# Optimization experiments

Hardware: AMD Instinct MI355X
Metric: run time of the kernel (lower is better)

Reference implementation:

```python
import jax, jax.numpy as jnp
import numpy as np

D_MODEL = 512
N_HEADS = 8
D_K = D_MODEL // N_HEADS
D_EDGE = 16
D_FF = 2048
B, N = 4, 1024
LN_EPS = 1e-5


def layer_norm(x, g, b):
    mu = jnp.mean(x, axis=-1, keepdims=True)
    var = jnp.var(x, axis=-1, keepdims=True)
    return (x - mu) * jax.lax.rsqrt(var + LN_EPS) * g + b


def setup_inputs() -> dict:
    key = jax.random.key(0)
    ks = jax.random.split(key, 16)
    s = 0.02
    return {
        "x": jax.random.normal(ks[0], (B, N, D_MODEL), jnp.float32),
        "edge_emb": jax.random.normal(ks[1], (B, N, N, D_EDGE), jnp.float32),
        "mask": jnp.ones((B, N), dtype=bool),
        # attention weights (torch Linear layout: [out, in])
        "wq": jax.random.normal(ks[2], (D_MODEL, D_MODEL), jnp.float32) * s,
        "wk": jax.random.normal(ks[3], (D_MODEL, D_MODEL), jnp.float32) * s,
        "wv": jax.random.normal(ks[4], (D_MODEL, D_MODEL), jnp.float32) * s,
        "wo": jax.random.normal(ks[5], (D_MODEL, D_MODEL), jnp.float32) * s,
        "wo_b": jnp.zeros((D_MODEL,), jnp.float32),
        # edge bias projector
        "we": jax.random.normal(ks[6], (N_HEADS, D_EDGE), jnp.float32) * s,
        "we_b": jnp.zeros((N_HEADS,), jnp.float32),
        # layer norms
        "g1": jnp.ones((D_MODEL,), jnp.float32),
        "b1n": jnp.zeros((D_MODEL,), jnp.float32),
        "g2": jnp.ones((D_MODEL,), jnp.float32),
        "b2n": jnp.zeros((D_MODEL,), jnp.float32),
        # FFN
        "w1": jax.random.normal(ks[7], (D_FF, D_MODEL), jnp.float32) * s,
        "b1": jnp.zeros((D_FF,), jnp.float32),
        "w2": jax.random.normal(ks[8], (D_MODEL, D_FF), jnp.float32) * s,
        "b2": jnp.zeros((D_MODEL,), jnp.float32),
    }


def reference(x, edge_emb, mask, wq, wk, wv, wo, wo_b, we, we_b,
              g1, b1n, g2, b2n, w1, b1, w2, b2):
    Bx, n, D = x.shape
    H, d_k = N_HEADS, D // N_HEADS
    residual = x
    xn = layer_norm(x, g1, b1n)
    # [B, H, n, d_k]
    Q = (xn @ wq.T).reshape(Bx, n, H, d_k).transpose(0, 2, 1, 3)
    K = (xn @ wk.T).reshape(Bx, n, H, d_k).transpose(0, 2, 1, 3)
    V = (xn @ wv.T).reshape(Bx, n, H, d_k).transpose(0, 2, 1, 3)
    scale = 1.0 / jnp.sqrt(jnp.asarray(d_k, x.dtype))
    attn = jnp.einsum('bhid,bhjd->bhij', Q, K) * scale  # [B, H, n, n]
    # per-head additive edge bias: [B, n, n, H] -> [B, H, n, n]
    bias = (edge_emb @ we.T + we_b).transpose(0, 3, 1, 2)
    attn = attn + bias
    attn = jnp.where(mask[:, None, None, :], attn, -jnp.inf)
    attn = jax.nn.softmax(attn, axis=-1)
    attn = jnp.nan_to_num(attn, nan=0.0)  # fully-masked rows -> 0
    out = jnp.einsum('bhij,bhjd->bhid', attn, V)
    out = out.transpose(0, 2, 1, 3).reshape(Bx, n, D)
    out = out @ wo.T + wo_b
    x = residual + out
    xn2 = layer_norm(x, g2, b2n)
    h = jax.nn.gelu(xn2 @ w1.T + b1, approximate=False)  # torch nn.GELU default = exact
    x = x + (h @ w2.T + b2)
    return x
```

## Files before the change

### kernel.cpp

```cpp
#include <hip/hip_runtime.h>
#include <math.h>

#define D_MODEL 512
#define N_HEADS 8
#define D_K     64
#define D_EDGE  16
#define D_FF    2048
#define B_SZ    4
#define N_SEQ   1024
#define M_ROWS  (B_SZ * N_SEQ)
#define LN_EPS  1e-5f
#define JSPLIT  4
#define ROWS_T  (B_SZ * N_HEADS * N_SEQ)

typedef __attribute__((ext_vector_type(4))) float f32x4;
typedef __attribute__((ext_vector_type(8))) short s16x8;
typedef __attribute__((ext_vector_type(8))) unsigned short u16x8;
typedef __attribute__((ext_vector_type(4))) unsigned short u16x4;

__device__ __forceinline__ unsigned short f2bf(float f) {
  union { float f; unsigned u; } x; x.f = f;
  unsigned r = x.u + 0x7fffu + ((x.u >> 16) & 1u);
  return (unsigned short)(r >> 16);
}
__device__ __forceinline__ float bf2f(unsigned short u) {
  union { unsigned u; float f; } x; x.u = ((unsigned)u) << 16;
  return x.f;
}
__device__ __forceinline__ float gelu_exact(float v) {
  return 0.5f * v * (1.0f + erff(v * 0.70710678118654752440f));
}

__global__ __launch_bounds__(256) void cast_weights(
    const float* __restrict__ wq, const float* __restrict__ wk, const float* __restrict__ wv,
    const float* __restrict__ wo, const float* __restrict__ w1, const float* __restrict__ w2,
    unsigned short* __restrict__ wbf)
{
  const int i4 = blockIdx.x * 256 + threadIdx.x;
  const float* src; int off4;
  if (i4 < 196608) {
    const int sub = i4 >> 16;
    src = (sub == 0) ? wq : ((sub == 1) ? wk : wv);
    off4 = i4 & 65535;
  } else if (i4 < 262144) { src = wo; off4 = i4 - 196608; }
  else if (i4 < 524288)   { src = w1; off4 = i4 - 262144; }
  else                    { src = w2; off4 = i4 - 524288; }
  const float4 v = ((const float4*)src)[off4];
  u16x4 p = { f2bf(v.x), f2bf(v.y), f2bf(v.z), f2bf(v.w) };
  *(u16x4*)(wbf + (size_t)i4 * 4) = p;
}

__global__ __launch_bounds__(256) void ln_kernel(
    const float* __restrict__ x, const float* __restrict__ g,
    const float* __restrict__ bb, unsigned short* __restrict__ out)
{
  const int row  = blockIdx.x * 4 + (threadIdx.x >> 6);
  const int lane = threadIdx.x & 63;
  const float4* xr = (const float4*)(x + (size_t)row * D_MODEL);
  float4 v0 = xr[lane * 2 + 0];
  float4 v1 = xr[lane * 2 + 1];
  float s  = v0.x + v0.y + v0.z + v0.w + v1.x + v1.y + v1.z + v1.w;
  float ss = v0.x*v0.x + v0.y*v0.y + v0.z*v0.z + v0.w*v0.w
           + v1.x*v1.x + v1.y*v1.y + v1.z*v1.z + v1.w*v1.w;
  #pragma unroll
  for (int off = 32; off >= 1; off >>= 1) {
    s  += __shfl_xor(s, off);
    ss += __shfl_xor(ss, off);
  }
  const float mu  = s * (1.0f / D_MODEL);
  const float var = ss * (1.0f / D_MODEL) - mu * mu;
  const float r   = rsqrtf(var + LN_EPS);
  const float4* gp = (const float4*)g;
  const float4* bp = (const float4*)bb;
  float4 g0 = gp[lane*2+0], g1v = gp[lane*2+1];
  float4 b0 = bp[lane*2+0], b1v = bp[lane*2+1];
  u16x4 oa = { f2bf((v0.x - mu) * r * g0.x + b0.x),
               f2bf((v0.y - mu) * r * g0.y + b0.y),
               f2bf((v0.z - mu) * r * g0.z + b0.z),
               f2bf((v0.w - mu) * r * g0.w + b0.w) };
  u16x4 ob = { f2bf((v1.x - mu) * r * g1v.x + b1v.x),
               f2bf((v1.y - mu) * r * g1v.y + b1v.y),
               f2bf((v1.z - mu) * r * g1v.z + b1v.z),
               f2bf((v1.w - mu) * r * g1v.w + b1v.w) };
  unsigned short* orow = out + (size_t)row * D_MODEL + lane * 8;
  *(u16x4*)(orow)     = oa;
  *(u16x4*)(orow + 4) = ob;
}

template<int ACT, int RES, int OBF, int HB>
__global__ __launch_bounds__(256, 4) void gemm_bf16(
    const unsigned short* __restrict__ A, const unsigned short* __restrict__ W,
    const float* __restrict__ bias, const float* __restrict__ res,
    void* __restrict__ Cv, int Nout, int K)
{
  __shared__ unsigned short As[128 * 64];
  __shared__ unsigned short Ws[64 * 64];
  const int tid  = threadIdx.x;
  const int w    = tid >> 6;
  const int lane = tid & 63;
  const int g    = lane >> 4;
  const int c    = lane & 15;
  const int row0 = blockIdx.x * 128;
  const int col0 = blockIdx.y * 64;
  const f32x4 z = { 0.f, 0.f, 0.f, 0.f };
  f32x4 acc[2][4];
  #pragma unroll
  for (int fm = 0; fm < 2; ++fm)
    #pragma unroll
    for (int fn = 0; fn < 4; ++fn) acc[fm][fn] = z;

  for (int k0 = 0; k0 < K; k0 += 64) {
    #pragma unroll
    for (int i = 0; i < 4; ++i) {
      const int flat = i * 256 + tid;
      __builtin_amdgcn_global_load_lds(
          (const __attribute__((address_space(1))) void*)(A + (size_t)(row0 + (flat >> 3)) * K + k0 + (flat & 7) * 8),
          (__attribute__((address_space(3))) void*)(&As[flat * 8]), 16, 0, 0);
    }
    #pragma unroll
    for (int i = 0; i < 2; ++i) {
      const int flat = i * 256 + tid;
      __builtin_amdgcn_global_load_lds(
          (const __attribute__((address_space(1))) void*)(W + (size_t)(col0 + (flat >> 3)) * K + k0 + (flat & 7) * 8),
          (__attribute__((address_space(3))) void*)(&Ws[flat * 8]), 16, 0, 0);
    }
    __syncthreads();
    #pragma unroll
    for (int kk = 0; kk < 2; ++kk) {
      const s16x8 a0 = *(const s16x8*)&As[(w * 32 + c) * 64 + kk * 32 + 8 * g];
      const s16x8 a1 = *(const s16x8*)&As[(w * 32 + 16 + c) * 64 + kk * 32 + 8 * g];
      #pragma unroll
      for (int fn = 0; fn < 4; ++fn) {
        const s16x8 bfr = *(const s16x8*)&Ws[(fn * 16 + c) * 64 + kk * 32 + 8 * g];
        acc[0][fn] = __builtin_amdgcn_mfma_f32_16x16x32_bf16(a0, bfr, acc[0][fn], 0, 0, 0);
        acc[1][fn] = __builtin_amdgcn_mfma_f32_16x16x32_bf16(a1, bfr, acc[1][fn], 0, 0, 0);
      }
    }
    __syncthreads();
  }

  #pragma unroll
  for (int fn = 0; fn < 4; ++fn) {
    const int cc = col0 + fn * 16 + c;
    const float bv = HB ? bias[cc] : 0.0f;
    #pragma unroll
    for (int fm = 0; fm < 2; ++fm) {
      #pragma unroll
      for (int r = 0; r < 4; ++r) {
        const int rr = row0 + w * 32 + fm * 16 + 4 * g + r;
        float v = acc[fm][fn][r] + bv;
        if (ACT) v = gelu_exact(v);
        if (RES) v += res[(size_t)rr * Nout + cc];
        if (OBF) ((unsigned short*)Cv)[(size_t)rr * Nout + cc] = f2bf(v);
        else     ((float*)Cv)[(size_t)rr * Nout + cc] = v;
      }
    }
  }
}

__global__ __launch_bounds__(256) void transpose_v(
    const unsigned short* __restrict__ qkv, unsigned short* __restrict__ vT)
{
  const int bid = blockIdx.x;
  const int jt = bid & 15, h = (bid >> 4) & 7, b = bid >> 7;
  __shared__ unsigned short t[64][72];
  const int tid = threadIdx.x;
  #pragma unroll
  for (int itr = 0; itr < 2; ++itr) {
    const int flat = itr * 256 + tid;
    const int j = flat >> 3, ch = flat & 7;
    *(u16x8*)&t[j][ch * 8] =
        *(const u16x8*)(qkv + (size_t)(b * 1024 + jt * 64 + j) * 1536 + 1024 + h * 64 + ch * 8);
  }
  __syncthreads();
  #pragma unroll
  for (int itr = 0; itr < 2; ++itr) {
    const int flat = itr * 256 + tid;
    const int dd = flat >> 3, ch = flat & 7;
    u16x8 v;
    #pragma unroll
    for (int e = 0; e < 8; ++e) v[e] = t[ch * 8 + e][dd];
    *(u16x8*)(vT + (size_t)((b * 8 + h) * 64 + dd) * 1024 + jt * 64 + ch * 8) = v;
  }
}

__global__ __launch_bounds__(512, 4) void attn_kernel(
    const unsigned short* __restrict__ qkv, const unsigned short* __restrict__ vT,
    const float* __restrict__ edge, const unsigned char* __restrict__ mask,
    const float* __restrict__ we, const float* __restrict__ web,
    float* __restrict__ pm, float* __restrict__ pl, float* __restrict__ pacc)
{
  __shared__ unsigned short bias_s[8][32][40];
  __shared__ unsigned short p_s[8][32][40];
  __shared__ float we_s[8][16];
  __shared__ float web_s[8];

  const int bid   = blockIdx.x;
  const int b     = (bid & 7) >> 1;
  const int local = ((bid >> 3) << 1) | (bid & 1);
  const int split = local & 3;
  const int it    = local >> 2;
  const int i0    = it * 32;
  const int tid   = threadIdx.x;
  const int h     = tid >> 6;
  const int lane  = tid & 63;
  const int g     = lane >> 4;
  const int c     = lane & 15;

  if (tid < 128) we_s[tid >> 4][tid & 15] = we[tid];
  if (tid < 8)   web_s[tid] = web[tid];

  s16x8 qf[2][2];
  #pragma unroll
  for (int fm = 0; fm < 2; ++fm)
    #pragma unroll
    for (int kk = 0; kk < 2; ++kk)
      qf[fm][kk] = *(const s16x8*)(qkv + (size_t)(b * 1024 + i0 + fm * 16 + c) * 1536 + h * 64 + kk * 32 + 8 * g);

  const f32x4 z = { 0.f, 0.f, 0.f, 0.f };
  f32x4 o[2][4];
  #pragma unroll
  for (int fm = 0; fm < 2; ++fm)
    #pragma unroll
    for (int fd = 0; fd < 4; ++fd) o[fm][fd] = z;
  float mreg[2][4], lreg[2][4];
  #pragma unroll
  for (int fm = 0; fm < 2; ++fm)
    #pragma unroll
    for (int r = 0; r < 4; ++r) { mreg[fm][r] = -1e30f; lreg[fm][r] = 0.f; }

  for (int jc = 0; jc < 8; ++jc) {
    const int j0 = split * 256 + jc * 32;
    __syncthreads();
    {
      const int pi  = tid >> 4;
      const int pjb = (tid & 15) * 2;
      #pragma unroll
      for (int pp = 0; pp < 2; ++pp) {
        const int pj = pjb + pp;
        const int j  = j0 + pj;
        const float4* ep = (const float4*)(edge +
            ((((size_t)b * N_SEQ) + (i0 + pi)) * N_SEQ + j) * D_EDGE);
        const float4 e0 = ep[0], e1 = ep[1], e2 = ep[2], e3 = ep[3];
        const float mk = mask[b * N_SEQ + j] ? 0.0f : -1e30f;
        #pragma unroll
        for (int hh = 0; hh < 8; ++hh) {
          const float* wv = we_s[hh];
          const float d =
              e0.x*wv[0]  + e0.y*wv[1]  + e0.z*wv[2]  + e0.w*wv[3]
            + e1.x*wv[4]  + e1.y*wv[5]  + e1.z*wv[6]  + e1.w*wv[7]
            + e2.x*wv[8]  + e2.y*wv[9]  + e2.z*wv[10] + e2.w*wv[11]
            + e3.x*wv[12] + e3.y*wv[13] + e3.z*wv[14] + e3.w*wv[15];
          bias_s[hh][pi][pj] = f2bf(d + web_s[hh] + mk);
        }
      }
    }
    __syncthreads();

    f32x4 s[2][2];
    s[0][0] = z; s[0][1] = z; s[1][0] = z; s[1][1] = z;
    #pragma unroll
    for (int fn = 0; fn < 2; ++fn)
      #pragma unroll
      for (int kk = 0; kk < 2; ++kk) {
        const s16x8 kf = *(const s16x8*)(qkv +
            (size_t)(b * 1024 + j0 + fn * 16 + c) * 1536 + 512 + h * 64 + kk * 32 + 8 * g);
        #pragma unroll
        for (int fm = 0; fm < 2; ++fm)
          s[fm][fn] = __builtin_amdgcn_mfma_f32_16x16x32_bf16(qf[fm][kk], kf, s[fm][fn], 0, 0, 0);
      }

    #pragma unroll
    for (int fm = 0; fm < 2; ++fm) {
      #pragma unroll
      for (int r = 0; r < 4; ++r) {
        const int irow = fm * 16 + 4 * g + r;
        const float s0 = s[fm][0][r] * 0.125f + bf2f(bias_s[h][irow][c]);
        const float s1 = s[fm][1][r] * 0.125f + bf2f(bias_s[h][irow][16 + c]);
        float v = fmaxf(s0, s1);
        v = fmaxf(v, __shfl_xor(v, 1));
        v = fmaxf(v, __shfl_xor(v, 2));
        v = fmaxf(v, __shfl_xor(v, 4));
        v = fmaxf(v, __shfl_xor(v, 8));
        const float nm    = fmaxf(mreg[fm][r], v);
        const float alpha = __expf(mreg[fm][r] - nm);
        mreg[fm][r] = nm;
        const float p0 = __expf(s0 - nm);
        const float p1 = __expf(s1 - nm);
        lreg[fm][r] = lreg[fm][r] * alpha + p0 + p1;
        #pragma unroll
        for (int fd = 0; fd < 4; ++fd) o[fm][fd][r] *= alpha;
        p_s[h][irow][c]      = f2bf(p0);
        p_s[h][irow][16 + c] = f2bf(p1);
      }
    }

    s16x8 pa[2];
    #pragma unroll
    for (int fm = 0; fm < 2; ++fm)
      pa[fm] = *(const s16x8*)&p_s[h][fm * 16 + c][8 * g];
    #pragma unroll
    for (int fd = 0; fd < 4; ++fd) {
      const s16x8 vf = *(const s16x8*)(vT +
          (size_t)((b * 8 + h) * 64 + fd * 16 + c) * 1024 + j0 + 8 * g);
      #pragma unroll
      for (int fm = 0; fm < 2; ++fm)
        o[fm][fd] = __builtin_amdgcn_mfma_f32_16x16x32_bf16(pa[fm], vf, o[fm][fd], 0, 0, 0);
    }
  }

  #pragma unroll
  for (int fm = 0; fm < 2; ++fm) {
    #pragma unroll
    for (int r = 0; r < 4; ++r) {
      float lv = lreg[fm][r];
      lv += __shfl_xor(lv, 1);
      lv += __shfl_xor(lv, 2);
      lv += __shfl_xor(lv, 4);
      lv += __shfl_xor(lv, 8);
      const int row = ((split * B_SZ + b) * N_HEADS + h) * N_SEQ + i0 + fm * 16 + 4 * g + r;
      #pragma unroll
      for (int fd = 0; fd < 4; ++fd)
        pacc[(size_t)row * 64 + fd * 16 + c] = o[fm][fd][r];
      if (c == 0) { pm[row] = mreg[fm][r]; pl[row] = lv; }
    }
  }
}

__global__ __launch_bounds__(256) void merge_kernel(
    const float* __restrict__ pm, const float* __restrict__ pl,
    const float* __restrict__ pacc, unsigned short* __restrict__ ao)
{
  const int row = blockIdx.x * 4 + (threadIdx.x >> 6);
  const int d   = threadIdx.x & 63;
  float ms[JSPLIT], ls[JSPLIT];
  float M = -3e38f;
  #pragma unroll
  for (int s2 = 0; s2 < JSPLIT; ++s2) {
    ms[s2] = pm[s2 * ROWS_T + row];
    ls[s2] = pl[s2 * ROWS_T + row];
    M = fmaxf(M, ms[s2]);
  }
  float acc = 0.f, inv = 0.f;
  if (M > -1e29f) {
    float L = 0.f;
    #pragma unroll
    for (int s2 = 0; s2 < JSPLIT; ++s2) {
      const float wgt = __expf(ms[s2] - M);
      L += ls[s2] * wgt;
      acc += wgt * pacc[((size_t)s2 * ROWS_T + row) * 64 + d];
    }
    inv = 1.0f / L;
  }
  const int b2 = row >> 13, h2 = (row >> 10) & 7, i2 = row & 1023;
  ao[(size_t)(b2 * 1024 + i2) * 512 + h2 * 64 + d] = f2bf(acc * inv);
}

extern "C" void kernel_launch(void* const* d_in, const int* in_sizes, int n_in,
                              void* d_out, int out_size, void* d_ws, size_t ws_size,
                              hipStream_t stream) {
  const float* x    = (const float*)d_in[0];
  const float* edge = (const float*)d_in[1];
  const unsigned char* mask = (const unsigned char*)d_in[2];
  const float* wq   = (const float*)d_in[3];
  const float* wk   = (const float*)d_in[4];
  const float* wv   = (const float*)d_in[5];
  const float* wo   = (const float*)d_in[6];
  const float* wo_b = (const float*)d_in[7];
  const float* we   = (const float*)d_in[8];
  const float* we_b = (const float*)d_in[9];
  const float* g1   = (const float*)d_in[10];
  const float* b1n  = (const float*)d_in[11];
  const float* g2   = (const float*)d_in[12];
  const float* b2n  = (const float*)d_in[13];
  const float* w1   = (const float*)d_in[14];
  const float* b1   = (const float*)d_in[15];
  const float* w2   = (const float*)d_in[16];
  const float* b2   = (const float*)d_in[17];
  float* out = (float*)d_out;
  char* ws = (char*)d_ws;

  const size_t MB = 1048576;
  unsigned short* xn_bf  = (unsigned short*)(ws + 0 * MB);
  unsigned short* qkv_bf = (unsigned short*)(ws + 4 * MB);
  unsigned short* vT     = (unsigned short*)(ws + 16 * MB);
  unsigned short* ao_bf  = (unsigned short*)(ws + 20 * MB);
  float*          x2     = (float*)(ws + 24 * MB);
  unsigned short* wbf    = (unsigned short*)(ws + 32 * MB);
  float*          pm     = (float*)(ws + 38 * MB);
  float*          pl     = (float*)(ws + 38 * MB + 524288);
  float*          pacc   = (float*)(ws + 41 * MB);
  unsigned short* hbuf   = (unsigned short*)(ws + 41 * MB);

  unsigned short* wqkv_bf = wbf;
  unsigned short* wo_bf   = wbf + 786432;
  unsigned short* w1_bf   = wbf + 1048576;
  unsigned short* w2_bf   = wbf + 2097152;

  cast_weights<<<3072, 256, 0, stream>>>(wq, wk, wv, wo, w1, w2, wbf);
  ln_kernel<<<M_ROWS / 4, 256, 0, stream>>>(x, g1, b1n, xn_bf);
  {
    dim3 grid(M_ROWS / 128, 1536 / 64);
    gemm_bf16<0, 0, 1, 0><<<grid, 256, 0, stream>>>(xn_bf, wqkv_bf, nullptr, nullptr, qkv_bf, 1536, 512);
  }
  transpose_v<<<512, 256, 0, stream>>>(qkv_bf, vT);
  attn_kernel<<<512, 512, 0, stream>>>(qkv_bf, vT, edge, mask, we, we_b, pm, pl, pacc);
  merge_kernel<<<ROWS_T / 4, 256, 0, stream>>>(pm, pl, pacc, ao_bf);
  {
    dim3 grid(M_ROWS / 128, 512 / 64);
    gemm_bf16<0, 1, 0, 1><<<grid, 256, 0, stream>>>(ao_bf, wo_bf, wo_b, x, (void*)x2, 512, 512);
  }
  ln_kernel<<<M_ROWS / 4, 256, 0, stream>>>(x2, g2, b2n, xn_bf);
  {
    dim3 grid(M_ROWS / 128, 2048 / 64);
    gemm_bf16<1, 0, 1, 1><<<grid, 256, 0, stream>>>(xn_bf, w1_bf, b1, nullptr, hbuf, 2048, 512);
  }
  {
    dim3 grid(M_ROWS / 128, 512 / 64);
    gemm_bf16<0, 1, 0, 1><<<grid, 256, 0, stream>>>(hbuf, w2_bf, b2, x2, (void*)out, 512, 2048);
  }
}
```

Before: 587.4 us.

## Halve attention row tile, prefetch edge features, add 64x64 GEMM for narrow outputs

The attention kernel now handles 16 query rows per block instead of 32, doubling the grid to 1024 blocks. The next chunk's edge embedding is prefetched into registers while the current chunk is processed, and the jc loop is fully unrolled. A new 64x64-tile GEMM using global_load_lds feeds the two 512-wide output projections (Wo and W2) to raise block count and occupancy. In exchange, per-block K/V reuse drops in attention and the new GEMM has no double-buffering.

After: 587.9 us. Within noise of the previous version (+0.1%).

```diff
diff --git a/kernel.cpp b/kernel.cpp
--- a/kernel.cpp
+++ b/kernel.cpp
@@ -158,6 +158,76 @@
   }
 }
 
+template<int ACT, int RES, int OBF, int HB>
+__global__ __launch_bounds__(256, 4) void gemm64_bf16(
+    const unsigned short* __restrict__ A, const unsigned short* __restrict__ W,
+    const float* __restrict__ bias, const float* __restrict__ res,
+    void* __restrict__ Cv, int Nout, int K)
+{
+  __shared__ unsigned short As[64 * 64];
+  __shared__ unsigned short Ws[64 * 64];
+  const int tid  = threadIdx.x;
+  const int w    = tid >> 6;
+  const int lane = tid & 63;
+  const int g    = lane >> 4;
+  const int c    = lane & 15;
+  const int wr   = (w >> 1) * 32;
+  const int wc   = (w & 1) * 32;
+  const int row0 = blockIdx.x * 64;
+  const int col0 = blockIdx.y * 64;
+  const f32x4 z = { 0.f, 0.f, 0.f, 0.f };
+  f32x4 acc[2][2];
+  acc[0][0] = z; acc[0][1] = z; acc[1][0] = z; acc[1][1] = z;
+
+  for (int k0 = 0; k0 < K; k0 += 64) {
+    #pragma unroll
+    for (int i = 0; i < 2; ++i) {
+      const int flat = i * 256 + tid;
+      __builtin_amdgcn_global_load_lds(
+          (const __attribute__((address_space(1))) void*)(A + (size_t)(row0 + (flat >> 3)) * K + k0 + (flat & 7) * 8),
+          (__attribute__((address_space(3))) void*)(&As[flat * 8]), 16, 0, 0);
+    }
+    #pragma unroll
+    for (int i = 0; i < 2; ++i) {
+      const int flat = i * 256 + tid;
+      __builtin_amdgcn_global_load_lds(
+          (const __attribute__((address_space(1))) void*)(W + (size_t)(col0 + (flat >> 3)) * K + k0 + (flat & 7) * 8),
+          (__attribute__((address_space(3))) void*)(&Ws[flat * 8]), 16, 0, 0);
+    }
+    __syncthreads();
+    #pragma unroll
+    for (int kk = 0; kk < 2; ++kk) {
+      const s16x8 a0 = *(const s16x8*)&As[(wr + c) * 64 + kk * 32 + 8 * g];
+      const s16x8 a1 = *(const s16x8*)&As[(wr + 16 + c) * 64 + kk * 32 + 8 * g];
+      #pragma unroll
+      for (int fn = 0; fn < 2; ++fn) {
+        const s16x8 bfr = *(const s16x8*)&Ws[(wc + fn * 16 + c) * 64 + kk * 32 + 8 * g];
+        acc[0][fn] = __builtin_amdgcn_mfma_f32_16x16x32_bf16(a0, bfr, acc[0][fn], 0, 0, 0);
+        acc[1][fn] = __builtin_amdgcn_mfma_f32_16x16x32_bf16(a1, bfr, acc[1][fn], 0, 0, 0);
+      }
+    }
+    __syncthreads();
+  }
+
+  #pragma unroll
+  for (int fn = 0; fn < 2; ++fn) {
+    const int cc = col0 + wc + fn * 16 + c;
+    const float bv = HB ? bias[cc] : 0.0f;
+    #pragma unroll
+    for (int fm = 0; fm < 2; ++fm) {
+      #pragma unroll
+      for (int r = 0; r < 4; ++r) {
+        const int rr = row0 + wr + fm * 16 + 4 * g + r;
+        float v = acc[fm][fn][r] + bv;
+        if (ACT) v = gelu_exact(v);
+        if (RES) v += res[(size_t)rr * Nout + cc];
+        if (OBF) ((unsigned short*)Cv)[(size_t)rr * Nout + cc] = f2bf(v);
+        else     ((float*)Cv)[(size_t)rr * Nout + cc] = v;
+      }
+    }
+  }
+}
+
 __global__ __launch_bounds__(256) void transpose_v(
     const unsigned short* __restrict__ qkv, unsigned short* __restrict__ vT)
 {
@@ -190,140 +260,128 @@
     const float* __restrict__ we, const float* __restrict__ web,
     float* __restrict__ pm, float* __restrict__ pl, float* __restrict__ pacc)
 {
-  __shared__ unsigned short bias_s[8][32][40];
-  __shared__ unsigned short p_s[8][32][40];
+  __shared__ unsigned short bias_s[8][16][40];
+  __shared__ unsigned short p_s[8][16][40];
   __shared__ float we_s[8][16];
   __shared__ float web_s[8];
 
   const int bid   = blockIdx.x;
-  const int b     = (bid & 7) >> 1;
-  const int local = ((bid >> 3) << 1) | (bid & 1);
-  const int split = local & 3;
-  const int it    = local >> 2;
-  const int i0    = it * 32;
+  const int split = bid & 3;
+  const int it    = (bid >> 2) & 63;
+  const int b     = bid >> 8;
+  const int i0    = it * 16;
   const int tid   = threadIdx.x;
   const int h     = tid >> 6;
   const int lane  = tid & 63;
   const int g     = lane >> 4;
   const int c     = lane & 15;
+  const int pi    = tid >> 5;
+  const int pj    = tid & 31;
+  const int j0b   = split * 256;
 
   if (tid < 128) we_s[tid >> 4][tid & 15] = we[tid];
   if (tid < 8)   web_s[tid] = web[tid];
 
-  s16x8 qf[2][2];
-  #pragma unroll
-  for (int fm = 0; fm < 2; ++fm)
-    #pragma unroll
-    for (int kk = 0; kk < 2; ++kk)
-      qf[fm][kk] = *(const s16x8*)(qkv + (size_t)(b * 1024 + i0 + fm * 16 + c) * 1536 + h * 64 + kk * 32 + 8 * g);
+  s16x8 qf[2];
+  #pragma unroll
+  for (int kk = 0; kk < 2; ++kk)
+    qf[kk] = *(const s16x8*)(qkv + (size_t)(b * 1024 + i0 + c) * 1536 + h * 64 + kk * 32 + 8 * g);
 
   const f32x4 z = { 0.f, 0.f, 0.f, 0.f };
-  f32x4 o[2][4];
-  #pragma unroll
-  for (int fm = 0; fm < 2; ++fm)
-    #pragma unroll
-    for (int fd = 0; fd < 4; ++fd) o[fm][fd] = z;
-  float mreg[2][4], lreg[2][4];
-  #pragma unroll
-  for (int fm = 0; fm < 2; ++fm)
-    #pragma unroll
-    for (int r = 0; r < 4; ++r) { mreg[fm][r] = -1e30f; lreg[fm][r] = 0.f; }
-
+  f32x4 o[4];
+  #pragma unroll
+  for (int fd = 0; fd < 4; ++fd) o[fd] = z;
+  float mreg[4], lreg[4];
+  #pragma unroll
+  for (int r = 0; r < 4; ++r) { mreg[r] = -1e30f; lreg[r] = 0.f; }
+
+  float4 er[4];
+  {
+    const float4* ep = (const float4*)(edge +
+        ((((size_t)b << 10) + (i0 + pi)) * 1024 + (j0b + pj)) * 16);
+    er[0] = ep[0]; er[1] = ep[1]; er[2] = ep[2]; er[3] = ep[3];
+  }
+
+  #pragma unroll
   for (int jc = 0; jc < 8; ++jc) {
-    const int j0 = split * 256 + jc * 32;
-    __syncthreads();
+    const int j0 = j0b + jc * 32;
+    __syncthreads();
+
     {
-      const int pi  = tid >> 4;
-      const int pjb = (tid & 15) * 2;
-      #pragma unroll
-      for (int pp = 0; pp < 2; ++pp) {
-        const int pj = pjb + pp;
-        const int j  = j0 + pj;
-        const float4* ep = (const float4*)(edge +
-            ((((size_t)b * N_SEQ) + (i0 + pi)) * N_SEQ + j) * D_EDGE);
-        const float4 e0 = ep[0], e1 = ep[1], e2 = ep[2], e3 = ep[3];
-        const float mk = mask[b * N_SEQ + j] ? 0.0f : -1e30f;
-        #pragma unroll
-        for (int hh = 0; hh < 8; ++hh) {
-          const float* wv = we_s[hh];
-          const float d =
-              e0.x*wv[0]  + e0.y*wv[1]  + e0.z*wv[2]  + e0.w*wv[3]
-            + e1.x*wv[4]  + e1.y*wv[5]  + e1.z*wv[6]  + e1.w*wv[7]
-            + e2.x*wv[8]  + e2.y*wv[9]  + e2.z*wv[10] + e2.w*wv[11]
-            + e3.x*wv[12] + e3.y*wv[13] + e3.z*wv[14] + e3.w*wv[15];
-          bias_s[hh][pi][pj] = f2bf(d + web_s[hh] + mk);
-        }
-      }
-    }
-    __syncthreads();
-
-    f32x4 s[2][2];
-    s[0][0] = z; s[0][1] = z; s[1][0] = z; s[1][1] = z;
+      const float mk = mask[(b << 10) + j0 + pj] ? 0.0f : -1e30f;
+      #pragma unroll
+      for (int hh = 0; hh < 8; ++hh) {
+        const float* wv = we_s[hh];
+        const float d =
+            er[0].x*wv[0]  + er[0].y*wv[1]  + er[0].z*wv[2]  + er[0].w*wv[3]
+          + er[1].x*wv[4]  + er[1].y*wv[5]  + er[1].z*wv[6]  + er[1].w*wv[7]
+          + er[2].x*wv[8]  + er[2].y*wv[9]  + er[2].z*wv[10] + er[2].w*wv[11]
+          + er[3].x*wv[12] + er[3].y*wv[13] + er[3].z*wv[14] + er[3].w*wv[15];
+        bias_s[hh][pi][pj] = f2bf(d + web_s[hh] + mk);
+      }
+    }
+    __syncthreads();
+
+    if (jc < 7) {
+      const float4* ep = (const float4*)(edge +
+          ((((size_t)b << 10) + (i0 + pi)) * 1024 + (j0 + 32 + pj)) * 16);
+      er[0] = ep[0]; er[1] = ep[1]; er[2] = ep[2]; er[3] = ep[3];
+    }
+
+    f32x4 s[2];
+    s[0] = z; s[1] = z;
     #pragma unroll
     for (int fn = 0; fn < 2; ++fn)
       #pragma unroll
       for (int kk = 0; kk < 2; ++kk) {
         const s16x8 kf = *(const s16x8*)(qkv +
             (size_t)(b * 1024 + j0 + fn * 16 + c) * 1536 + 512 + h * 64 + kk * 32 + 8 * g);
-        #pragma unroll
-        for (int fm = 0; fm < 2; ++fm)
-          s[fm][fn] = __builtin_amdgcn_mfma_f32_16x16x32_bf16(qf[fm][kk], kf, s[fm][fn], 0, 0, 0);
-      }
-
-    #pragma unroll
-    for (int fm = 0; fm < 2; ++fm) {
-      #pragma unroll
-      for (int r = 0; r < 4; ++r) {
-        const int irow = fm * 16 + 4 * g + r;
-        const float s0 = s[fm][0][r] * 0.125f + bf2f(bias_s[h][irow][c]);
-        const float s1 = s[fm][1][r] * 0.125f + bf2f(bias_s[h][irow][16 + c]);
-        float v = fmaxf(s0, s1);
-        v = fmaxf(v, __shfl_xor(v, 1));
-        v = fmaxf(v, __shfl_xor(v, 2));
-        v = fmaxf(v, __shfl_xor(v, 4));
-        v = fmaxf(v, __shfl_xor(v, 8));
-        const float nm    = fmaxf(mreg[fm][r], v);
-        const float alpha = __expf(mreg[fm][r] - nm);
-        mreg[fm][r] = nm;
-        const float p0 = __expf(s0 - nm);
-        const float p1 = __expf(s1 - nm);
-        lreg[fm][r] = lreg[fm][r] * alpha + p0 + p1;
-        #pragma unroll
-        for (int fd = 0; fd < 4; ++fd) o[fm][fd][r] *= alpha;
-        p_s[h][irow][c]      = f2bf(p0);
-        p_s[h][irow][16 + c] = f2bf(p1);
-      }
-    }
-
-    s16x8 pa[2];
-    #pragma unroll
-    for (int fm = 0; fm < 2; ++fm)
-      pa[fm] = *(const s16x8*)&p_s[h][fm * 16 + c][8 * g];
+        s[fn] = __builtin_amdgcn_mfma_f32_16x16x32_bf16(qf[kk], kf, s[fn], 0, 0, 0);
+      }
+
+    #pragma unroll
+    for (int r = 0; r < 4; ++r) {
+      const int irow = 4 * g + r;
+      const float s0 = s[0][r] * 0.125f + bf2f(bias_s[h][irow][c]);
+      const float s1 = s[1][r] * 0.125f + bf2f(bias_s[h][irow][16 + c]);
+      float v = fmaxf(s0, s1);
+      v = fmaxf(v, __shfl_xor(v, 1));
+      v = fmaxf(v, __shfl_xor(v, 2));
+      v = fmaxf(v, __shfl_xor(v, 4));
+      v = fmaxf(v, __shfl_xor(v, 8));
+      const float nm    = fmaxf(mreg[r], v);
+      const float alpha = __expf(mreg[r] - nm);
+      mreg[r] = nm;
+      const float p0 = __expf(s0 - nm);
+      const float p1 = __expf(s1 - nm);
+      lreg[r] = lreg[r] * alpha + p0 + p1;
+      #pragma unroll
+      for (int fd = 0; fd < 4; ++fd) o[fd][r] *= alpha;
+      p_s[h][irow][c]      = f2bf(p0);
+      p_s[h][irow][16 + c] = f2bf(p1);
+    }
+
+    const s16x8 pa = *(const s16x8*)&p_s[h][c][8 * g];
     #pragma unroll
     for (int fd = 0; fd < 4; ++fd) {
       const s16x8 vf = *(const s16x8*)(vT +
           (size_t)((b * 8 + h) * 64 + fd * 16 + c) * 1024 + j0 + 8 * g);
-      #pragma unroll
-      for (int fm = 0; fm < 2; ++fm)
-        o[fm][fd] = __builtin_amdgcn_mfma_f32_16x16x32_bf16(pa[fm], vf, o[fm][fd], 0, 0, 0);
-    }
-  }
-
-  #pragma unroll
-  for (int fm = 0; fm < 2; ++fm) {
-    #pragma unroll
-    for (int r = 0; r < 4; ++r) {
-      float lv = lreg[fm][r];
-      lv += __shfl_xor(lv, 1);
-      lv += __shfl_xor(lv, 2);
-      lv += __shfl_xor(lv, 4);
-      lv += __shfl_xor(lv, 8);
-      const int row = ((split * B_SZ + b) * N_HEADS + h) * N_SEQ + i0 + fm * 16 + 4 * g + r;
-      #pragma unroll
-      for (int fd = 0; fd < 4; ++fd)
-        pacc[(size_t)row * 64 + fd * 16 + c] = o[fm][fd][r];
-      if (c == 0) { pm[row] = mreg[fm][r]; pl[row] = lv; }
-    }
+      o[fd] = __builtin_amdgcn_mfma_f32_16x16x32_bf16(pa, vf, o[fd], 0, 0, 0);
+    }
+  }
+
+  #pragma unroll
+  for (int r = 0; r < 4; ++r) {
+    float lv = lreg[r];
+    lv += __shfl_xor(lv, 1);
+    lv += __shfl_xor(lv, 2);
+    lv += __shfl_xor(lv, 4);
+    lv += __shfl_xor(lv, 8);
+    const int row = ((split * B_SZ + b) * N_HEADS + h) * N_SEQ + i0 + 4 * g + r;
+    #pragma unroll
+    for (int fd = 0; fd < 4; ++fd)
+      pacc[(size_t)row * 64 + fd * 16 + c] = o[fd][r];
+    if (c == 0) { pm[row] = mreg[r]; pl[row] = lv; }
   }
 }
 
@@ -404,11 +462,11 @@
     gemm_bf16<0, 0, 1, 0><<<grid, 256, 0, stream>>>(xn_bf, wqkv_bf, nullptr, nullptr, qkv_bf, 1536, 512);
   }
   transpose_v<<<512, 256, 0, stream>>>(qkv_bf, vT);
-  attn_kernel<<<512, 512, 0, stream>>>(qkv_bf, vT, edge, mask, we, we_b, pm, pl, pacc);
+  attn_kernel<<<1024, 512, 0, stream>>>(qkv_bf, vT, edge, mask, we, we_b, pm, pl, pacc);
   merge_kernel<<<ROWS_T / 4, 256, 0, stream>>>(pm, pl, pacc, ao_bf);
   {
-    dim3 grid(M_ROWS / 128, 512 / 64);
-    gemm_bf16<0, 1, 0, 1><<<grid, 256, 0, stream>>>(ao_bf, wo_bf, wo_b, x, (void*)x2, 512, 512);
+    dim3 grid(M_ROWS / 64, 512 / 64);
+    gemm64_bf16<0, 1, 0, 1><<<grid, 256, 0, stream>>>(ao_bf, wo_bf, wo_b, x, (void*)x2, 512, 512);
   }
   ln_kernel<<<M_ROWS / 4, 256, 0, stream>>>(x2, g2, b2n, xn_bf);
   {
@@ -416,7 +474,7 @@
     gemm_bf16<1, 0, 1, 1><<<grid, 256, 0, stream>>>(xn_bf, w1_bf, b1, nullptr, hbuf, 2048, 512);
   }
   {
-    dim3 grid(M_ROWS / 128, 512 / 64);
-    gemm_bf16<0, 1, 0, 1><<<grid, 256, 0, stream>>>(hbuf, w2_bf, b2, x2, (void*)out, 512, 2048);
-  }
-}
+    dim3 grid(M_ROWS / 64, 512 / 64);
+    gemm64_bf16<0, 1, 0, 1><<<grid, 256, 0, stream>>>(hbuf, w2_bf, b2, x2, (void*)out, 512, 2048);
+  }
+}
```
